# Optimization experiments

Measured on AMD Instinct MI355X. Metric: run time of the kernel, lower is better.

## Reference

```python
import jax, jax.numpy as jnp
import numpy as np

N_NODES = 40000
N_EDGES = 640000
IN_CH = 128
HID_CH = 128
BN_EPS = 1e-5


def setup_inputs() -> dict:
    key = jax.random.key(0)
    k_x, k_ei, k_w, k_g = jax.random.split(key, 4)
    x = jax.random.normal(k_x, (N_NODES, IN_CH), dtype=jnp.float32)
    edge_index = jax.random.randint(k_ei, (2, N_EDGES), 0, N_NODES, dtype=jnp.int32)
    # Glorot init for GCNConv weight, zero bias (PyG defaults)
    limit = float(np.sqrt(6.0 / (IN_CH + HID_CH)))
    W = jax.random.uniform(k_w, (IN_CH, HID_CH), dtype=jnp.float32, minval=-limit, maxval=limit)
    b = jnp.zeros((HID_CH,), dtype=jnp.float32)
    gamma = jnp.ones((HID_CH,), dtype=jnp.float32)
    beta = jnp.zeros((HID_CH,), dtype=jnp.float32)
    return {"x": x, "edge_index": edge_index, "W": W, "b": b, "gamma": gamma, "beta": beta}


def reference(x, edge_index, W, b, gamma, beta):
    N = x.shape[0]
    src, dst = edge_index[0], edge_index[1]

    # --- GCNConv: h = x @ W, symmetric-normalized aggregation with self-loops ---
    h = x @ W  # [N, H]
    ones = jnp.ones((src.shape[0],), dtype=x.dtype)
    deg = jax.ops.segment_sum(ones, dst, num_segments=N) + 1.0  # +1 for self-loop
    dinv = jax.lax.rsqrt(deg)  # deg >= 1 always
    norm = dinv[src] * dinv[dst]  # [E]
    msg = h[src] * norm[:, None]  # [E, H] gather
    agg = jax.ops.segment_sum(msg, dst, num_segments=N)  # scatter-add
    agg = agg + h * (dinv * dinv)[:, None]  # self-loop contribution
    out = agg + b  # bias added after aggregation (PyG GCNConv)

    # --- BatchNorm1d (training mode: batch stats, biased variance) ---
    mean = jnp.mean(out, axis=0)
    var = jnp.mean((out - mean) ** 2, axis=0)
    out = gamma * (out - mean) * jax.lax.rsqrt(var + BN_EPS) + beta

    # --- ReLU (dropout is a no-op in eval) ---
    return jax.nn.relu(out)
```

## Files before the change

kernel.cpp:

```cpp
#include <hip/hip_runtime.h>

#define N_NODES 40000
#define N_EDGES 640000
#define CH 128
#define BN_EPS 1e-5f
#define CAP 64
#define MM_ROWS 160
#define MM_BLOCKS (N_NODES / MM_ROWS)
#define FILL_BLOCKS (N_EDGES / 1024)


typedef __bf16 bf16x8 __attribute__((ext_vector_type(8)));
typedef float f32x4 __attribute__((ext_vector_type(4)));

__device__ __forceinline__ float bf_lo(unsigned u) { return __uint_as_float(u << 16); }
__device__ __forceinline__ float bf_hi(unsigned u) { return __uint_as_float(u & 0xffff0000u); }
__device__ __forceinline__ unsigned short f2bf(float f) {
    unsigned u = __float_as_uint(f);
    unsigned r = 0x7fffu + ((u >> 16) & 1u);
    return (unsigned short)((u + r) >> 16);
}
__device__ __forceinline__ unsigned pack2bf(float a, float b) {
    return (unsigned)f2bf(a) | ((unsigned)f2bf(b) << 16);
}

__global__ __launch_bounds__(256) void mm_fill_kernel(const float* __restrict__ x,
                                                      const float* __restrict__ W,
                                                      unsigned short* __restrict__ hbf,
                                                      const int* __restrict__ src,
                                                      const int* __restrict__ dst,
                                                      int* __restrict__ cnt,
                                                      unsigned short* __restrict__ bucket16) {
    __shared__ uint4 Wsb4[2048];
    int t = threadIdx.x;
    int bb = blockIdx.x;
    if (bb >= MM_BLOCKS) {
        int fi = bb - MM_BLOCKS;
        int base = cnt[N_NODES];
        int4 dd = ((const int4*)dst)[fi * 256 + t];
        int4 ss = ((const int4*)src)[fi * 256 + t];
        int d[4] = {dd.x, dd.y, dd.z, dd.w};
        int s[4] = {ss.x, ss.y, ss.z, ss.w};
#pragma unroll
        for (int k = 0; k < 4; ++k) {
            int slot = atomicAdd(&cnt[d[k]], 1) - base;
            if (slot < CAP) bucket16[d[k] * CAP + slot] = (unsigned short)s[k];
        }
        return;
    }
#pragma unroll
    for (int it = 0; it < 8; ++it) {
        int task = it * 256 + t;
        int n = task & 127;
        int k8 = task >> 7;
        const float* wp = W + (size_t)(k8 * 8) * CH + n;
        float w0 = wp[0 * CH], w1 = wp[1 * CH], w2 = wp[2 * CH], w3 = wp[3 * CH];
        float w4 = wp[4 * CH], w5 = wp[5 * CH], w6 = wp[6 * CH], w7 = wp[7 * CH];
        uint4 u;
        u.x = pack2bf(w0, w1); u.y = pack2bf(w2, w3);
        u.z = pack2bf(w4, w5); u.w = pack2bf(w6, w7);
        int ks = k8 >> 2, q = k8 & 3, ct = n >> 4;
        Wsb4[(ct * 4 + ks) * 64 + q * 16 + (n & 15)] = u;
    }
    __syncthreads();
    int w = t >> 6, l = t & 63;
    int q = l >> 4, c15 = l & 15;
    int ct0 = 2 * w, ct1 = 2 * w + 1;
    bf16x8 bf0[4], bf1[4];
#pragma unroll
    for (int ks = 0; ks < 4; ++ks) {
        bf0[ks] = __builtin_bit_cast(bf16x8, Wsb4[(ct0 * 4 + ks) * 64 + l]);
        bf1[ks] = __builtin_bit_cast(bf16x8, Wsb4[(ct1 * 4 + ks) * 64 + l]);
    }
    size_t row0 = (size_t)bb * MM_ROWS;
    for (int rt = 0; rt < MM_ROWS / 16; ++rt) {
        const float4* xr = (const float4*)(x + (row0 + rt * 16 + c15) * CH);
        float4 xf[8];
#pragma unroll
        for (int ks = 0; ks < 4; ++ks) {
            xf[2 * ks]     = xr[ks * 8 + 2 * q];
            xf[2 * ks + 1] = xr[ks * 8 + 2 * q + 1];
        }
        f32x4 acc0 = {0.f, 0.f, 0.f, 0.f};
        f32x4 acc1 = {0.f, 0.f, 0.f, 0.f};
#pragma unroll
        for (int ks = 0; ks < 4; ++ks) {
            float4 f0 = xf[2 * ks], f1 = xf[2 * ks + 1];
            uint4 ua;
            ua.x = pack2bf(f0.x, f0.y); ua.y = pack2bf(f0.z, f0.w);
            ua.z = pack2bf(f1.x, f1.y); ua.w = pack2bf(f1.z, f1.w);
            bf16x8 af = __builtin_bit_cast(bf16x8, ua);
            acc0 = __builtin_amdgcn_mfma_f32_16x16x32_bf16(af, bf0[ks], acc0, 0, 0, 0);
            acc1 = __builtin_amdgcn_mfma_f32_16x16x32_bf16(af, bf1[ks], acc1, 0, 0, 0);
        }
        unsigned short* hr = hbf + (row0 + rt * 16 + q * 4) * CH;
#pragma unroll
        for (int r = 0; r < 4; ++r) {
            hr[r * CH + ct0 * 16 + c15] = f2bf(acc0[r]);
            hr[r * CH + ct1 * 16 + c15] = f2bf(acc1[r]);
        }
    }
}

__global__ __launch_bounds__(256) void aggregate_kernel(const unsigned short* __restrict__ bucket16,
                                                        const int* __restrict__ cnt,
                                                        const unsigned short* __restrict__ hbf,
                                                        const float* __restrict__ b,
                                                        float* __restrict__ out,
                                                        float* __restrict__ sums32) {
    __shared__ float bsum[CH], bsq[CH];
    int t = threadIdx.x;
    if (t < CH) { bsum[t] = 0.0f; bsq[t] = 0.0f; }
    __syncthreads();
    int base = cnt[N_NODES];
    int wid = t >> 6;
    int lane = t & 63;
    int quarter = lane >> 4;
    int ql = lane & 15;
    const uint4* h4 = (const uint4*)hbf;
    float4 bv0 = ((const float4*)b)[ql * 2];
    float4 bv1 = ((const float4*)b)[ql * 2 + 1];
    int n_base = blockIdx.x * 16 + wid * 4;
    float s0 = 0, s1 = 0, s2 = 0, s3 = 0, s4 = 0, s5 = 0, s6 = 0, s7 = 0;
    float q0 = 0, q1 = 0, q2 = 0, q3 = 0, q4 = 0, q5 = 0, q6 = 0, q7 = 0;
#pragma unroll 1
    for (int it = 0; it < 4; ++it) {
        int n = n_base + it;
        int cn = cnt[n] - base;
        int m = cn < CAP ? cn : CAP;
        float dn = rsqrtf((float)cn + 1.0f);
        unsigned sx_pre = (lane < m) ? (unsigned)bucket16[n * CAP + lane] : 0u;
        float a0 = 0, a1 = 0, a2 = 0, a3 = 0, a4 = 0, a5 = 0, a6 = 0, a7 = 0;
        for (int jj = 0; jj < m; jj += 16) {
            int e = jj + quarter * 4;
            unsigned sx0 = (unsigned)__shfl((int)sx_pre, e, 64);
            unsigned sx1 = (unsigned)__shfl((int)sx_pre, e + 1, 64);
            unsigned sx2 = (unsigned)__shfl((int)sx_pre, e + 2, 64);
            unsigned sx3 = (unsigned)__shfl((int)sx_pre, e + 3, 64);
            int c0g = cnt[sx0];
            int c1g = cnt[sx1];
            int c2g = cnt[sx2];
            int c3g = cnt[sx3];
            uint4 r0 = h4[(size_t)sx0 * 16 + ql];
            uint4 r1 = h4[(size_t)sx1 * 16 + ql];
            uint4 r2 = h4[(size_t)sx2 * 16 + ql];
            uint4 r3 = h4[(size_t)sx3 * 16 + ql];
            float d0 = (e     < m) ? rsqrtf((float)(c0g - base) + 1.0f) : 0.0f;
            float d1 = (e + 1 < m) ? rsqrtf((float)(c1g - base) + 1.0f) : 0.0f;
            float d2 = (e + 2 < m) ? rsqrtf((float)(c2g - base) + 1.0f) : 0.0f;
            float d3 = (e + 3 < m) ? rsqrtf((float)(c3g - base) + 1.0f) : 0.0f;
            a0 += bf_lo(r0.x) * d0; a1 += bf_hi(r0.x) * d0;
            a2 += bf_lo(r0.y) * d0; a3 += bf_hi(r0.y) * d0;
            a4 += bf_lo(r0.z) * d0; a5 += bf_hi(r0.z) * d0;
            a6 += bf_lo(r0.w) * d0; a7 += bf_hi(r0.w) * d0;
            a0 += bf_lo(r1.x) * d1; a1 += bf_hi(r1.x) * d1;
            a2 += bf_lo(r1.y) * d1; a3 += bf_hi(r1.y) * d1;
            a4 += bf_lo(r1.z) * d1; a5 += bf_hi(r1.z) * d1;
            a6 += bf_lo(r1.w) * d1; a7 += bf_hi(r1.w) * d1;
            a0 += bf_lo(r2.x) * d2; a1 += bf_hi(r2.x) * d2;
            a2 += bf_lo(r2.y) * d2; a3 += bf_hi(r2.y) * d2;
            a4 += bf_lo(r2.z) * d2; a5 += bf_hi(r2.z) * d2;
            a6 += bf_lo(r2.w) * d2; a7 += bf_hi(r2.w) * d2;
            a0 += bf_lo(r3.x) * d3; a1 += bf_hi(r3.x) * d3;
            a2 += bf_lo(r3.y) * d3; a3 += bf_hi(r3.y) * d3;
            a4 += bf_lo(r3.z) * d3; a5 += bf_hi(r3.z) * d3;
            a6 += bf_lo(r3.w) * d3; a7 += bf_hi(r3.w) * d3;
        }
        a0 += __shfl_xor(a0, 16, 64); a0 += __shfl_xor(a0, 32, 64);
        a1 += __shfl_xor(a1, 16, 64); a1 += __shfl_xor(a1, 32, 64);
        a2 += __shfl_xor(a2, 16, 64); a2 += __shfl_xor(a2, 32, 64);
        a3 += __shfl_xor(a3, 16, 64); a3 += __shfl_xor(a3, 32, 64);
        a4 += __shfl_xor(a4, 16, 64); a4 += __shfl_xor(a4, 32, 64);
        a5 += __shfl_xor(a5, 16, 64); a5 += __shfl_xor(a5, 32, 64);
        a6 += __shfl_xor(a6, 16, 64); a6 += __shfl_xor(a6, 32, 64);
        a7 += __shfl_xor(a7, 16, 64); a7 += __shfl_xor(a7, 32, 64);
        if (quarter == 0) {
            uint4 raw = h4[(size_t)n * 16 + ql];
            float sq = dn * dn;
            float o0 = a0 * dn + bf_lo(raw.x) * sq + bv0.x;
            float o1 = a1 * dn + bf_hi(raw.x) * sq + bv0.y;
            float o2 = a2 * dn + bf_lo(raw.y) * sq + bv0.z;
            float o3 = a3 * dn + bf_hi(raw.y) * sq + bv0.w;
            float o4 = a4 * dn + bf_lo(raw.z) * sq + bv1.x;
            float o5 = a5 * dn + bf_hi(raw.z) * sq + bv1.y;
            float o6 = a6 * dn + bf_lo(raw.w) * sq + bv1.z;
            float o7 = a7 * dn + bf_hi(raw.w) * sq + bv1.w;
            float4* op = (float4*)(out + (size_t)n * CH + ql * 8);
            float4 w0 = {o0, o1, o2, o3};
            float4 w1 = {o4, o5, o6, o7};
            op[0] = w0;
            op[1] = w1;
            s0 += o0; q0 += o0 * o0;
            s1 += o1; q1 += o1 * o1;
            s2 += o2; q2 += o2 * o2;
            s3 += o3; q3 += o3 * o3;
            s4 += o4; q4 += o4 * o4;
            s5 += o5; q5 += o5 * o5;
            s6 += o6; q6 += o6 * o6;
            s7 += o7; q7 += o7 * o7;
        }
    }
    if (quarter == 0) {
        int c0 = ql * 8;
        atomicAdd(&bsum[c0 + 0], s0); atomicAdd(&bsq[c0 + 0], q0);
        atomicAdd(&bsum[c0 + 1], s1); atomicAdd(&bsq[c0 + 1], q1);
        atomicAdd(&bsum[c0 + 2], s2); atomicAdd(&bsq[c0 + 2], q2);
        atomicAdd(&bsum[c0 + 3], s3); atomicAdd(&bsq[c0 + 3], q3);
        atomicAdd(&bsum[c0 + 4], s4); atomicAdd(&bsq[c0 + 4], q4);
        atomicAdd(&bsum[c0 + 5], s5); atomicAdd(&bsq[c0 + 5], q5);
        atomicAdd(&bsum[c0 + 6], s6); atomicAdd(&bsq[c0 + 6], q6);
        atomicAdd(&bsum[c0 + 7], s7); atomicAdd(&bsq[c0 + 7], q7);
    }
    __syncthreads();
    atomicAdd(&sums32[(blockIdx.x & 31) * 256 + t], (t < CH) ? bsum[t] : bsq[t - CH]);
}

__global__ __launch_bounds__(256) void bn_relu_kernel(float* __restrict__ out,
                                                      const float* __restrict__ sums32,
                                                      const float* __restrict__ gamma,
                                                      const float* __restrict__ beta) {
    __shared__ float sc[CH], sh[CH];
    int t = threadIdx.x;
    if (t < CH) {
        float P = sums32[32 * 256];
        float s = -32.0f * P, q = -32.0f * P;
#pragma unroll
        for (int k = 0; k < 32; ++k) {
            s += sums32[k * 256 + t];
            q += sums32[k * 256 + CH + t];
        }
        const float invN = 1.0f / (float)N_NODES;
        float mean = s * invN;
        float var = q * invN - mean * mean;
        float scale = gamma[t] * rsqrtf(var + BN_EPS);
        sc[t] = scale;
        sh[t] = beta[t] - mean * scale;
    }
    __syncthreads();
    int i = blockIdx.x * 256 + t;
    int c0 = (i & 31) * 4;
    float4 v = ((float4*)out)[i];
    float r0 = v.x * sc[c0] + sh[c0];
    float r1 = v.y * sc[c0 + 1] + sh[c0 + 1];
    float r2 = v.z * sc[c0 + 2] + sh[c0 + 2];
    float r3 = v.w * sc[c0 + 3] + sh[c0 + 3];
    v.x = r0 > 0.0f ? r0 : 0.0f;
    v.y = r1 > 0.0f ? r1 : 0.0f;
    v.z = r2 > 0.0f ? r2 : 0.0f;
    v.w = r3 > 0.0f ? r3 : 0.0f;
    ((float4*)out)[i] = v;
}

extern "C" void kernel_launch(void* const* d_in, const int* in_sizes, int n_in,
                              void* d_out, int out_size, void* d_ws, size_t ws_size,
                              hipStream_t stream) {
    const float* x = (const float*)d_in[0];
    const int* ei = (const int*)d_in[1];
    const float* W = (const float*)d_in[2];
    const float* b = (const float*)d_in[3];
    const float* gamma = (const float*)d_in[4];
    const float* beta = (const float*)d_in[5];
    float* out = (float*)d_out;
    const int* src = ei;
    const int* dst = ei + N_EDGES;
    char* ws = (char*)d_ws;

    unsigned short* hbf = (unsigned short*)ws;
    int* cnt = (int*)(ws + 10240000);
    float* sums32 = (float*)(ws + 10400256);
    unsigned short* bucket16 = (unsigned short*)(ws + 10433280);

    mm_fill_kernel<<<MM_BLOCKS + FILL_BLOCKS, 256, 0, stream>>>(x, W, hbf, src, dst, cnt,
                                                                bucket16);
    aggregate_kernel<<<N_NODES / 16, 256, 0, stream>>>(bucket16, cnt, hbf, b, out, sums32);
    bn_relu_kernel<<<N_NODES * CH / 4 / 256, 256, 0, stream>>>(out, sums32, gamma, beta);
}
```

Measured before the change: 165.1 us.

## Stage x tile in LDS as bf16, load W fragments directly, fill blocks first

```diff
diff --git a/kernel.cpp b/kernel.cpp
--- a/kernel.cpp
+++ b/kernel.cpp
@@ -5,7 +5,7 @@
 #define CH 128
 #define BN_EPS 1e-5f
 #define CAP 64
-#define MM_ROWS 160
+#define MM_ROWS 80
 #define MM_BLOCKS (N_NODES / MM_ROWS)
 #define FILL_BLOCKS (N_EDGES / 1024)
 
@@ -31,64 +31,64 @@
                                                       const int* __restrict__ dst,
                                                       int* __restrict__ cnt,
                                                       unsigned short* __restrict__ bucket16) {
-    __shared__ uint4 Wsb4[2048];
+    __shared__ unsigned xl[MM_ROWS * 68];
     int t = threadIdx.x;
     int bb = blockIdx.x;
-    if (bb >= MM_BLOCKS) {
-        int fi = bb - MM_BLOCKS;
+    if (bb < FILL_BLOCKS) {
         int base = cnt[N_NODES];
-        int4 dd = ((const int4*)dst)[fi * 256 + t];
-        int4 ss = ((const int4*)src)[fi * 256 + t];
+        int4 dd = ((const int4*)dst)[bb * 256 + t];
+        int4 ss = ((const int4*)src)[bb * 256 + t];
         int d[4] = {dd.x, dd.y, dd.z, dd.w};
         int s[4] = {ss.x, ss.y, ss.z, ss.w};
-#pragma unroll
-        for (int k = 0; k < 4; ++k) {
-            int slot = atomicAdd(&cnt[d[k]], 1) - base;
-            if (slot < CAP) bucket16[d[k] * CAP + slot] = (unsigned short)s[k];
-        }
+        int slot[4];
+#pragma unroll
+        for (int k = 0; k < 4; ++k) slot[k] = atomicAdd(&cnt[d[k]], 1) - base;
+#pragma unroll
+        for (int k = 0; k < 4; ++k)
+            if (slot[k] < CAP) bucket16[d[k] * CAP + slot[k]] = (unsigned short)s[k];
         return;
     }
-#pragma unroll
-    for (int it = 0; it < 8; ++it) {
-        int task = it * 256 + t;
-        int n = task & 127;
-        int k8 = task >> 7;
-        const float* wp = W + (size_t)(k8 * 8) * CH + n;
-        float w0 = wp[0 * CH], w1 = wp[1 * CH], w2 = wp[2 * CH], w3 = wp[3 * CH];
-        float w4 = wp[4 * CH], w5 = wp[5 * CH], w6 = wp[6 * CH], w7 = wp[7 * CH];
-        uint4 u;
-        u.x = pack2bf(w0, w1); u.y = pack2bf(w2, w3);
-        u.z = pack2bf(w4, w5); u.w = pack2bf(w6, w7);
-        int ks = k8 >> 2, q = k8 & 3, ct = n >> 4;
-        Wsb4[(ct * 4 + ks) * 64 + q * 16 + (n & 15)] = u;
-    }
-    __syncthreads();
+    int mb = bb - FILL_BLOCKS;
+    size_t row0 = (size_t)mb * MM_ROWS;
+#pragma unroll
+    for (int it = 0; it < MM_ROWS * 32 / 256; ++it) {
+        int idx = it * 256 + t;
+        int row = idx >> 5, c4 = idx & 31;
+        float4 f = ((const float4*)(x + (row0 + row) * CH))[c4];
+        uint2 p;
+        p.x = pack2bf(f.x, f.y);
+        p.y = pack2bf(f.z, f.w);
+        *(uint2*)&xl[row * 68 + 2 * c4] = p;
+    }
     int w = t >> 6, l = t & 63;
     int q = l >> 4, c15 = l & 15;
     int ct0 = 2 * w, ct1 = 2 * w + 1;
     bf16x8 bf0[4], bf1[4];
 #pragma unroll
     for (int ks = 0; ks < 4; ++ks) {
-        bf0[ks] = __builtin_bit_cast(bf16x8, Wsb4[(ct0 * 4 + ks) * 64 + l]);
-        bf1[ks] = __builtin_bit_cast(bf16x8, Wsb4[(ct1 * 4 + ks) * 64 + l]);
-    }
-    size_t row0 = (size_t)bb * MM_ROWS;
+        const float* wp = W + (size_t)(ks * 32 + 8 * q) * CH + c15;
+        float v0[8], v1[8];
+#pragma unroll
+        for (int j = 0; j < 8; ++j) {
+            v0[j] = wp[j * CH + ct0 * 16];
+            v1[j] = wp[j * CH + ct1 * 16];
+        }
+        uint4 u0, u1;
+        u0.x = pack2bf(v0[0], v0[1]); u0.y = pack2bf(v0[2], v0[3]);
+        u0.z = pack2bf(v0[4], v0[5]); u0.w = pack2bf(v0[6], v0[7]);
+        u1.x = pack2bf(v1[0], v1[1]); u1.y = pack2bf(v1[2], v1[3]);
+        u1.z = pack2bf(v1[4], v1[5]); u1.w = pack2bf(v1[6], v1[7]);
+        bf0[ks] = __builtin_bit_cast(bf16x8, u0);
+        bf1[ks] = __builtin_bit_cast(bf16x8, u1);
+    }
+    __syncthreads();
     for (int rt = 0; rt < MM_ROWS / 16; ++rt) {
-        const float4* xr = (const float4*)(x + (row0 + rt * 16 + c15) * CH);
-        float4 xf[8];
-#pragma unroll
-        for (int ks = 0; ks < 4; ++ks) {
-            xf[2 * ks]     = xr[ks * 8 + 2 * q];
-            xf[2 * ks + 1] = xr[ks * 8 + 2 * q + 1];
-        }
+        int rbase = rt * 16 + c15;
         f32x4 acc0 = {0.f, 0.f, 0.f, 0.f};
         f32x4 acc1 = {0.f, 0.f, 0.f, 0.f};
 #pragma unroll
         for (int ks = 0; ks < 4; ++ks) {
-            float4 f0 = xf[2 * ks], f1 = xf[2 * ks + 1];
-            uint4 ua;
-            ua.x = pack2bf(f0.x, f0.y); ua.y = pack2bf(f0.z, f0.w);
-            ua.z = pack2bf(f1.x, f1.y); ua.w = pack2bf(f1.z, f1.w);
+            uint4 ua = *(const uint4*)&xl[rbase * 68 + ks * 16 + 4 * q];
             bf16x8 af = __builtin_bit_cast(bf16x8, ua);
             acc0 = __builtin_amdgcn_mfma_f32_16x16x32_bf16(af, bf0[ks], acc0, 0, 0, 0);
             acc1 = __builtin_amdgcn_mfma_f32_16x16x32_bf16(af, bf1[ks], acc1, 0, 0, 0);
@@ -270,7 +270,7 @@
     float* sums32 = (float*)(ws + 10400256);
     unsigned short* bucket16 = (unsigned short*)(ws + 10433280);
 
-    mm_fill_kernel<<<MM_BLOCKS + FILL_BLOCKS, 256, 0, stream>>>(x, W, hbf, src, dst, cnt,
+    mm_fill_kernel<<<FILL_BLOCKS + MM_BLOCKS, 256, 0, stream>>>(x, W, hbf, src, dst, cnt,
                                                                 bucket16);
     aggregate_kernel<<<N_NODES / 16, 256, 0, stream>>>(bucket16, cnt, hbf, b, out, sums32);
     bn_relu_kernel<<<N_NODES * CH / 4 / 256, 256, 0, stream>>>(out, sums32, gamma, beta);
```

Result: faster. 158.8 us (-3.8%).
